# Optimization experiments

Measured on AMD Instinct MI355X. Metric: run time of the kernel, lower is better.

Reference implementation:

```python
import jax, jax.numpy as jnp
import numpy as np

D_MODEL = 2048
N_HEADS = 16
N_KV = 4
HEAD_DIM = 128
SUB = 64
WINDOW = 512
THETA = 10000.0
NEG = jnp.float32(-1e30)


def _rope_tables(seq_len):
    inv_freq = 1.0 / (THETA ** (jnp.arange(0, HEAD_DIM, 2, dtype=jnp.float32) / HEAD_DIM))
    freqs = jnp.arange(seq_len, dtype=jnp.float32)[:, None] * inv_freq[None, :]  # [S, hd/2]
    emb = jnp.concatenate([freqs, freqs], axis=-1)  # [S, hd]
    return jnp.cos(emb), jnp.sin(emb)


def _rotate_half(x):
    x1, x2 = x[..., : HEAD_DIM // 2], x[..., HEAD_DIM // 2 :]
    return jnp.concatenate([-x2, x1], axis=-1)


def _apply_rope(t, cos, sin):
    # t: [B, H, S, hd]; cos/sin: [S, hd]
    c = cos[None, None]
    s = sin[None, None]
    return t * c + _rotate_half(t) * s


def setup_inputs() -> dict:
    key = jax.random.key(0)
    ks = jax.random.split(key, 6)
    B, S = 1, 2048
    std = 0.02
    return {
        "x": jax.random.normal(ks[0], (B, S, D_MODEL), dtype=jnp.float32),
        "Wq": jax.random.normal(ks[1], (D_MODEL, N_HEADS * HEAD_DIM), dtype=jnp.float32) * std,
        "Wk": jax.random.normal(ks[2], (D_MODEL, N_KV * HEAD_DIM), dtype=jnp.float32) * std,
        "Wv": jax.random.normal(ks[3], (D_MODEL, N_KV * HEAD_DIM), dtype=jnp.float32) * std,
        "Wo": jax.random.normal(ks[4], (N_HEADS * HEAD_DIM, D_MODEL), dtype=jnp.float32) * std,
        "lam": jnp.full((N_HEADS,), 0.1, dtype=jnp.float32),
    }


def reference(x, Wq, Wk, Wv, Wo, lam):
    B, S, _ = x.shape
    n_rep = N_HEADS // N_KV

    q = (x @ Wq).reshape(B, S, N_HEADS, HEAD_DIM).transpose(0, 2, 1, 3)  # [B,H,S,hd]
    k = (x @ Wk).reshape(B, S, N_KV, HEAD_DIM).transpose(0, 2, 1, 3)    # [B,KH,S,hd]
    v = (x @ Wv).reshape(B, S, N_KV, HEAD_DIM).transpose(0, 2, 1, 3)

    cos, sin = _rope_tables(S)
    q = _apply_rope(q, cos, sin)
    k = _apply_rope(k, cos, sin)

    # GQA repeat: each kv head replicated n_rep times consecutively
    k = jnp.repeat(k, n_rep, axis=1)  # [B,H,S,hd]
    v = jnp.repeat(v, n_rep, axis=1)

    q1, q2 = q[..., :SUB], q[..., SUB:]
    k1, k2 = k[..., :SUB], k[..., SUB:]
    scale = 1.0 / jnp.sqrt(jnp.float32(SUB))

    s1 = jnp.einsum("bhqd,bhkd->bhqk", q1, k1) * scale
    s2 = jnp.einsum("bhqd,bhkd->bhqk", q2, k2) * scale

    i = jnp.arange(S)[:, None]
    j = jnp.arange(S)[None, :]
    allowed = (j <= i) & (j >= i - WINDOW + 1)  # causal + sliding window
    s1 = jnp.where(allowed[None, None], s1, NEG)
    s2 = jnp.where(allowed[None, None], s2, NEG)

    a1 = jax.nn.softmax(s1.astype(jnp.float32), axis=-1).astype(x.dtype)
    a2 = jax.nn.softmax(s2.astype(jnp.float32), axis=-1).astype(x.dtype)

    diff = jax.nn.relu(a1 - lam[None, :, None, None] * a2)
    diff = diff / (jnp.sum(diff, axis=-1, keepdims=True) + 1e-6)

    out = jnp.einsum("bhqk,bhkd->bhqd", diff, v)  # [B,H,S,hd]
    out = out.transpose(0, 2, 1, 3).reshape(B, S, N_HEADS * HEAD_DIM)
    return out @ Wo
```

## Files before the change

kernel.cpp:

```cpp
#include <hip/hip_runtime.h>
#include <hip/hip_bf16.h>
#include <stdint.h>

typedef __attribute__((ext_vector_type(8))) short short8;
typedef __attribute__((ext_vector_type(4))) float f32x4;
using bf16 = __hip_bfloat16;

#define MFMA16(a, b, c) __builtin_amdgcn_mfma_f32_16x16x32_bf16((a), (b), (c), 0, 0, 0)

#define GLOAD_LDS16(g, l) __builtin_amdgcn_global_load_lds( \
    (const __attribute__((address_space(1))) void*)(g),     \
    (__attribute__((address_space(3))) void*)(l), 16, 0, 0)

__device__ __forceinline__ unsigned packbf2(float lo, float hi) {
  unsigned r;
  asm("v_cvt_pk_bf16_f32 %0, %1, %2" : "=v"(r) : "v"(lo), "v"(hi));
  return r;
}
__device__ __forceinline__ float ex2(float x) {
  float r;
  asm("v_exp_f32 %0, %1" : "=v"(r) : "v"(x));
  return r;
}
__device__ __forceinline__ f32x4 vmax4(f32x4 a, f32x4 b) {
  f32x4 r;
  r[0] = fmaxf(a[0], b[0]); r[1] = fmaxf(a[1], b[1]);
  r[2] = fmaxf(a[2], b[2]); r[3] = fmaxf(a[3], b[3]);
  return r;
}

template <bool EDGE>
__device__ __forceinline__ void p1_update(const f32x4* sv, float& m, float& l,
                                          int kb0, int myq, int lhi) {
  f32x4 t4 = vmax4(vmax4(sv[0], sv[1]), vmax4(sv[2], sv[3]));
  float tm = fmaxf(fmaxf(t4[0], t4[1]), fmaxf(t4[2], t4[3]));
  float nm = fmaxf(m, tm);
  float sc = ex2(m - nm);
  float sum = 0.f;
#pragma unroll
  for (int nt = 0; nt < 4; ++nt) {
    float part = 0.f;
#pragma unroll
    for (int r = 0; r < 4; ++r) {
      float e = ex2(sv[nt][r] - nm);
      if (EDGE) {
        int key = kb0 + nt * 16 + lhi * 4 + r;
        bool ok = (key <= myq) && (key > myq - 512);
        e = ok ? e : 0.f;
      }
      part += e;
    }
    sum += part;
  }
  l = l * sc + sum;
  m = nm;
}

template <bool EDGE>
__device__ __forceinline__ float p2_probs(const f32x4* s1v, const f32x4* s2v,
                                          float m1, float m2, float c2,
                                          int kb0, int myq, int lhi, int l15,
                                          unsigned* pw) {
  float d0 = 0.f, d1 = 0.f;
#pragma unroll
  for (int nt = 0; nt < 4; ++nt) {
    float pr[4];
#pragma unroll
    for (int r = 0; r < 4; ++r) {
      float e1 = ex2(s1v[nt][r] - m1);
      float e2 = ex2(s2v[nt][r] - m2);
      float p = fmaf(-c2, e2, e1);
      p = fmaxf(p, 0.f);
      if (EDGE) {
        int key = kb0 + nt * 16 + lhi * 4 + r;
        bool ok = (key <= myq) && (key > myq - 512);
        p = ok ? p : 0.f;
      }
      pr[r] = p;
      if (r & 1) d1 += p; else d0 += p;
    }
    int pi = l15 * 36 + 8 * nt + 2 * lhi;
    pw[pi]     = packbf2(pr[0], pr[1]);
    pw[pi + 1] = packbf2(pr[2], pr[3]);
  }
  return d0 + d1;
}

__global__ __launch_bounds__(256) void prep_all(const float* __restrict__ x,
                                                const float* __restrict__ Wq,
                                                const float* __restrict__ Wk,
                                                const float* __restrict__ Wv,
                                                const float* __restrict__ Wo,
                                                bf16* __restrict__ xb,
                                                bf16* __restrict__ WqkvFT,
                                                bf16* __restrict__ WoFT)
{
  const int bx = blockIdx.x;
  const int tid = threadIdx.x;
  if (bx >= 80) {
    size_t i = ((size_t)(bx - 80) * 32 + blockIdx.y) * 2048 + tid * 8;
    const float* f = x + i;
    float4 a = *(const float4*)f;
    float4 b = *(const float4*)(f + 4);
    union { bf16 h[8]; short8 s; } u;
    u.h[0] = __float2bfloat16(a.x); u.h[1] = __float2bfloat16(a.y);
    u.h[2] = __float2bfloat16(a.z); u.h[3] = __float2bfloat16(a.w);
    u.h[4] = __float2bfloat16(b.x); u.h[5] = __float2bfloat16(b.y);
    u.h[6] = __float2bfloat16(b.z); u.h[7] = __float2bfloat16(b.w);
    *(short8*)(xb + i) = u.s;
    return;
  }
  const float* W;
  bf16* Wt;
  int N, n0;
  if (bx < 32)      { W = Wq; Wt = WqkvFT; N = 2048; n0 = bx * 64; }
  else if (bx < 40) { W = Wk; Wt = WqkvFT; N = 512;  n0 = 2048 + (bx - 32) * 64; }
  else if (bx < 48) { W = Wv; Wt = WqkvFT; N = 512;  n0 = 2560 + (bx - 40) * 64; }
  else              { W = Wo; Wt = WoFT;   N = 2048; n0 = (bx - 48) * 64; }
  const int nloc0 = (N == 512) ? (n0 - ((n0 >= 2560) ? 2560 : 2048)) : ((bx < 32 || bx >= 48) ? (n0 & 2047) : 0);
  const int k0 = blockIdx.y * 64;

  __shared__ bf16 t[64][72];
#pragma unroll
  for (int pass = 0; pass < 4; ++pass) {
    int r = pass * 16 + (tid >> 4);
    int c = (tid & 15) * 4;
    float4 v = *(const float4*)(W + (size_t)(k0 + r) * N + nloc0 + c);
    t[c + 0][r] = __float2bfloat16(v.x);
    t[c + 1][r] = __float2bfloat16(v.y);
    t[c + 2][r] = __float2bfloat16(v.z);
    t[c + 3][r] = __float2bfloat16(v.w);
  }
  __syncthreads();
#pragma unroll
  for (int pass = 0; pass < 2; ++pass) {
    int n = pass * 32 + (tid >> 3);
    int k8 = (tid & 7) * 8;
    int frag = ((n0 + n) >> 4) * 64 + ((k0 + k8) >> 5);
    int ln = (n & 15) + 16 * ((k8 >> 3) & 3);
    *(short8*)(Wt + (size_t)frag * 512 + ln * 8) = *(const short8*)(&t[n][k8]);
  }
}

__global__ __launch_bounds__(256) void transpose_v(const bf16* __restrict__ QKV,
                                                   bf16* __restrict__ VT)
{
  __shared__ bf16 t[64][72];
  const int tid = threadIdx.x;
  const int k0 = blockIdx.x * 64;
  const int d0 = blockIdx.y * 64;
#pragma unroll
  for (int pass = 0; pass < 2; ++pass) {
    int c = pass * 256 + tid;
    int r = c >> 3, cq = (c & 7) * 8;
    short8 v = *(const short8*)(QKV + (size_t)(k0 + r) * 3072 + 2560 + d0 + cq);
#pragma unroll
    for (int j = 0; j < 8; ++j) t[cq + j][r] = ((const bf16*)&v)[j];
  }
  __syncthreads();
#pragma unroll
  for (int pass = 0; pass < 2; ++pass) {
    int c = pass * 256 + tid;
    int d = c >> 3, kq = (c & 7) * 8;
    *(short8*)(VT + (size_t)(d0 + d) * 2048 + k0 + kq) = *(const short8*)(&t[d][kq]);
  }
}

template <int CF32>
__global__ __launch_bounds__(256) void gemm_ft(const bf16* __restrict__ A,
                                               const bf16* __restrict__ Bft,
                                               void* __restrict__ C,
                                               int M, int N, int K)
{
  __shared__ __align__(16) bf16 As[4][128 * 32];

  const int tid  = threadIdx.x;
  const int lane = tid & 63;
  const int w    = tid >> 6;
  const int wmg  = (w >> 1) * 4;
  const int wng  = (w & 1) * 4;
  const int l15  = lane & 15;
  const int lhi  = lane >> 4;
  const int bm0  = blockIdx.y * 128;
  const int bn0  = blockIdx.x * 128;

  const int srow = lane >> 2;
  const int scol = ((lane & 3) ^ ((lane >> 3) & 3)) * 8;
  const int loff = l15 * 4 + (lhi ^ ((l15 >> 1) & 3));

  const int nkc = K >> 5;
  const bf16* bbase[4];
#pragma unroll
  for (int nt = 0; nt < 4; ++nt)
    bbase[nt] = Bft + ((size_t)((bn0 >> 4) + wng + nt) * nkc) * 512 + lane * 8;

  f32x4 acc[4][4];
  const f32x4 zero4 = {0.f, 0.f, 0.f, 0.f};
#pragma unroll
  for (int i = 0; i < 4; ++i)
#pragma unroll
    for (int j = 0; j < 4; ++j) acc[i][j] = zero4;

  short8 br0[4], br1[4], br2[4], br3[4];

#define GSTAGE_A(buf, kk)                                                          \
  { _Pragma("unroll")                                                              \
    for (int p = 0; p < 2; ++p) {                                                  \
      int s   = (p * 4 + w) * 64 + lane;                                           \
      int row = (p * 4 + w) * 16 + srow;                                           \
      GLOAD_LDS16(A + (size_t)(bm0 + row) * K + (kk) + scol, &As[buf][s * 8]);     \
    } }

#define BLOAD(breg, kc)                                                            \
  { _Pragma("unroll")                                                              \
    for (int nt = 0; nt < 4; ++nt) {                                               \
      asm volatile("global_load_dwordx4 %0, %1, off"                               \
                   : "=v"(breg[nt])                                                \
                   : "v"(bbase[nt] + (size_t)(kc) * 512)                           \
                   : "memory");                                                    \
    } }

#define KSTEP(aslot, breg, wcn, ...)                                               \
  {                                                                                \
    asm volatile("s_waitcnt vmcnt(" #wcn ")" ::: "memory");                        \
    __builtin_amdgcn_s_barrier();                                                  \
    __builtin_amdgcn_sched_barrier(0);                                             \
    __VA_ARGS__                                                                    \
    short8 a_[4];                                                                  \
    _Pragma("unroll")                                                              \
    for (int mt = 0; mt < 4; ++mt)                                                 \
      a_[mt] = *(const short8*)(&As[aslot][((wmg + mt) * 64 + loff) * 8]);         \
    _Pragma("unroll")                                                              \
    for (int mt = 0; mt < 4; ++mt)                                                 \
      _Pragma("unroll")                                                            \
      for (int nt = 0; nt < 4; ++nt)                                               \
        acc[mt][nt] = MFMA16(a_[mt], breg[nt], acc[mt][nt]);                       \
  }

  GSTAGE_A(0, 0);  BLOAD(br0, 0);
  GSTAGE_A(1, 32); BLOAD(br1, 1);
  GSTAGE_A(2, 64); BLOAD(br2, 2);

  for (int t = 0; t < nkc - 4; t += 4) {
    KSTEP(0, br0, 12, GSTAGE_A(3, (t + 3) * 32); BLOAD(br3, t + 3);)
    KSTEP(1, br1, 12, GSTAGE_A(0, (t + 4) * 32); BLOAD(br0, t + 4);)
    KSTEP(2, br2, 12, GSTAGE_A(1, (t + 5) * 32); BLOAD(br1, t + 5);)
    KSTEP(3, br3, 12, GSTAGE_A(2, (t + 6) * 32); BLOAD(br2, t + 6);)
  }
  KSTEP(0, br0, 12, GSTAGE_A(3, (nkc - 1) * 32); BLOAD(br3, nkc - 1);)
  KSTEP(1, br1, 12, )
  KSTEP(2, br2, 6, )
  KSTEP(3, br3, 0, )

#undef GSTAGE_A
#undef BLOAD
#undef KSTEP

#pragma unroll
  for (int mt = 0; mt < 4; ++mt) {
    int row0 = bm0 + (wmg + mt) * 16 + lhi * 4;
#pragma unroll
    for (int nt = 0; nt < 4; ++nt) {
      int col = bn0 + (wng + nt) * 16 + l15;
#pragma unroll
      for (int r = 0; r < 4; ++r) {
        float val = acc[mt][nt][r];
        size_t idx = (size_t)(row0 + r) * N + col;
        if (CF32) ((float*)C)[idx] = val;
        else ((bf16*)C)[idx] = __float2bfloat16(val);
      }
    }
  }
}

__global__ __launch_bounds__(256) void rope2(bf16* __restrict__ QKV)
{
  const int NQ = 2048 * 16 * 8;
  int i = blockIdx.x * blockDim.x + threadIdx.x;
  bf16* base;
  int s, d0;
  float scale;
  if (i < NQ) {
    s = i >> 7;
    int rem = i & 127;
    int h = rem >> 3;
    d0 = (rem & 7) * 8;
    base = QKV + (size_t)s * 3072 + h * 128 + d0;
    scale = 0.180336880111120f;
  } else {
    int j = i - NQ;
    if (j >= 2048 * 4 * 8) return;
    s = j >> 5;
    int rem = j & 31;
    int h = rem >> 3;
    d0 = (rem & 7) * 8;
    base = QKV + (size_t)s * 3072 + 2048 + h * 128 + d0;
    scale = 1.f;
  }
  short8 x1v = *(const short8*)base;
  short8 x2v = *(const short8*)(base + 64);
  union { bf16 h[8]; short8 v; } o1, o2;
#pragma unroll
  for (int e = 0; e < 8; ++e) {
    float inv = __expf(-(float)(d0 + e) * (9.210340371976184f / 64.0f));
    float ang = (float)s * inv;
    float c = __cosf(ang), sn = __sinf(ang);
    union { short s; bf16 b; } u1, u2;
    u1.s = x1v[e]; u2.s = x2v[e];
    float x1 = __bfloat162float(u1.b);
    float x2 = __bfloat162float(u2.b);
    o1.h[e] = __float2bfloat16((x1 * c - x2 * sn) * scale);
    o2.h[e] = __float2bfloat16((x2 * c + x1 * sn) * scale);
  }
  *(short8*)base = o1.v;
  *(short8*)(base + 64) = o2.v;
}

__global__ __launch_bounds__(256) void diff_attn(const bf16* __restrict__ QKV,
                                                 const bf16* __restrict__ VT,
                                                 const float* __restrict__ lam,
                                                 bf16* __restrict__ O)
{
  __shared__ __align__(16) bf16 Kb[2][64 * 128];
  __shared__ __align__(16) bf16 Vb[2][128 * 64];
  __shared__ __align__(16) bf16 Pw[4][16 * 72];

  const int qb   = blockIdx.x;
  const int h    = blockIdx.y;
  const int kvh  = h >> 2;
  const int tid  = threadIdx.x;
  const int lane = tid & 63;
  const int w    = tid >> 6;
  const int l15  = lane & 15;
  const int lhi  = lane >> 4;
  const int qg   = qb * 64 + w * 16;
  const int myq  = qg + l15;
  const float lamv = lam[h];

  const bf16* Kg = QKV + 2048 + (size_t)kvh * 128;
  const bf16* Vg = VT + (size_t)kvh * 128 * 2048;

  short8 qf[4];
  {
    const bf16* qrow = QKV + (size_t)myq * 3072 + h * 128;
#pragma unroll
    for (int c = 0; c < 4; ++c)
      qf[c] = *(const short8*)(qrow + c * 32 + lhi * 8);
  }

  const int t0 = (qb >= 8) ? (qb - 8) : 0;

#define STAGE_K(buf, kbase)                                                     \
  {                                                                             \
    _Pragma("unroll")                                                           \
    for (int p = 0; p < 4; ++p) {                                               \
      int c = p * 256 + tid;                                                    \
      int r = c >> 4, q = c & 15;                                               \
      GLOAD_LDS16(Kg + (size_t)((kbase) + r) * 3072 + ((q ^ (r & 7)) * 8),      \
                  &Kb[buf][c * 8]);                                             \
    }                                                                           \
  }
#define STAGE_V(buf, kbase)                                                     \
  {                                                                             \
    _Pragma("unroll")                                                           \
    for (int p = 0; p < 4; ++p) {                                               \
      int c = p * 256 + tid;                                                    \
      int d = c >> 3, q = c & 7;                                                \
      GLOAD_LDS16(Vg + (size_t)d * 2048 + (kbase) + ((q ^ (d & 7)) * 8),        \
                  &Vb[buf][c * 8]);                                             \
    }                                                                           \
  }
#define KFRAG(buf, nt, qc) \
  (*(const short8*)(&Kb[buf][(((nt) * 16 + l15) * 16 + ((qc) ^ (((nt) * 16 + l15) & 7))) * 8]))
#define VFRAG(buf, n, qc) \
  (*(const short8*)(&Vb[buf][(((n) * 16 + l15) * 8 + ((qc) ^ (((n) * 16 + l15) & 7))) * 8]))
#define QK_TILE(cur)                                            \
  _Pragma("unroll")                                             \
  for (int nt = 0; nt < 4; ++nt) {                              \
    f32x4 s1 = zero4, s2 = zero4;                               \
    s1 = MFMA16(KFRAG(cur, nt, lhi),      qf[0], s1);           \
    s1 = MFMA16(KFRAG(cur, nt, 4 + lhi),  qf[1], s1);           \
    s2 = MFMA16(KFRAG(cur, nt, 8 + lhi),  qf[2], s2);           \
    s2 = MFMA16(KFRAG(cur, nt, 12 + lhi), qf[3], s2);           \
    s1v[nt] = s1; s2v[nt] = s2;                                 \
  }

  const f32x4 zero4 = {0.f, 0.f, 0.f, 0.f};

  float m1 = -1e30f, l1 = 0.f, m2 = -1e30f, l2 = 0.f;
  STAGE_K(0, t0 * 64);
  __syncthreads();
  {
    int cur = 0;
    for (int t = t0; t <= qb; ++t, cur ^= 1) {
      if (t < qb) STAGE_K(cur ^ 1, (t + 1) * 64);
      const int kb0 = t * 64;
      f32x4 s1v[4], s2v[4];
      QK_TILE(cur);
      const bool edge = (t == qb) || (qb >= 8 && t == t0);
      if (edge) {
        p1_update<true>(s1v, m1, l1, kb0, myq, lhi);
        p1_update<true>(s2v, m2, l2, kb0, myq, lhi);
      } else {
        p1_update<false>(s1v, m1, l1, kb0, myq, lhi);
        p1_update<false>(s2v, m2, l2, kb0, myq, lhi);
      }
      __syncthreads();
    }
  }

#pragma unroll
  for (int mk = 16; mk <= 32; mk <<= 1) {
    float pm = __shfl_xor(m1, mk, 64), pl = __shfl_xor(l1, mk, 64);
    float M = fmaxf(m1, pm);
    l1 = l1 * ex2(m1 - M) + pl * ex2(pm - M);
    m1 = M;
    pm = __shfl_xor(m2, mk, 64); pl = __shfl_xor(l2, mk, 64);
    M = fmaxf(m2, pm);
    l2 = l2 * ex2(m2 - M) + pl * ex2(pm - M);
    m2 = M;
  }
  const float c2 = lamv * l1 / l2;

  f32x4 accv[8];
#pragma unroll
  for (int n = 0; n < 8; ++n) accv[n] = zero4;
  float dln = 0.f;

  STAGE_K(0, t0 * 64);
  STAGE_V(0, t0 * 64);
  __syncthreads();
  {
    int cur = 0;
    for (int t = t0; t <= qb; ++t, cur ^= 1) {
      if (t < qb) {
        STAGE_K(cur ^ 1, (t + 1) * 64);
        STAGE_V(cur ^ 1, (t + 1) * 64);
      }
      const int kb0 = t * 64;
      unsigned* pw = (unsigned*)&Pw[w][0];
      f32x4 s1v[4], s2v[4];
      QK_TILE(cur);
      const bool edge = (t == qb) || (qb >= 8 && t == t0);
      if (edge) dln += p2_probs<true>(s1v, s2v, m1, m2, c2, kb0, myq, lhi, l15, pw);
      else      dln += p2_probs<false>(s1v, s2v, m1, m2, c2, kb0, myq, lhi, l15, pw);
#pragma unroll
      for (int kc = 0; kc < 2; ++kc) {
        short8 pa = *(const short8*)(&Pw[w][l15 * 72 + kc * 32 + lhi * 8]);
#pragma unroll
        for (int n = 0; n < 8; ++n)
          accv[n] = MFMA16(pa, VFRAG(cur, n, kc * 4 + lhi), accv[n]);
      }
      __syncthreads();
    }
  }

  dln += __shfl_xor(dln, 16, 64);
  dln += __shfl_xor(dln, 32, 64);

#pragma unroll
  for (int r = 0; r < 4; ++r) {
    int srcq = lhi * 4 + r;
    int src = (lane & 48) | srcq;
    float dq = __shfl(dln, src, 64);
    float lq = __shfl(l1, src, 64);
    float rinv = 1.f / (dq + lq * 1e-6f);
    int qo = qg + srcq;
#pragma unroll
    for (int n = 0; n < 8; ++n) {
      O[(size_t)qo * 2048 + h * 128 + n * 16 + l15] =
          __float2bfloat16(accv[n][r] * rinv);
    }
  }
#undef STAGE_K
#undef STAGE_V
#undef KFRAG
#undef VFRAG
#undef QK_TILE
}

extern "C" void kernel_launch(void* const* d_in, const int* in_sizes, int n_in,
                              void* d_out, int out_size, void* d_ws, size_t ws_size,
                              hipStream_t stream)
{
  const float* x   = (const float*)d_in[0];
  const float* Wq  = (const float*)d_in[1];
  const float* Wk  = (const float*)d_in[2];
  const float* Wv  = (const float*)d_in[3];
  const float* Wo  = (const float*)d_in[4];
  const float* lam = (const float*)d_in[5];

  char* ws = (char*)d_ws;
  bf16* xb     = (bf16*)(ws);
  bf16* WqkvFT = (bf16*)(ws + 8ull  * (1u << 20));
  bf16* WoFT   = (bf16*)(ws + 20ull * (1u << 20));
  bf16* QKV    = (bf16*)(ws + 28ull * (1u << 20));
  bf16* ATT    = (bf16*)(ws + 40ull * (1u << 20));
  bf16* VT     = (bf16*)(ws + 48ull * (1u << 20));

  prep_all<<<dim3(144, 32), 256, 0, stream>>>(x, Wq, Wk, Wv, Wo, xb, WqkvFT, WoFT);
  gemm_ft<0><<<dim3(24, 16), 256, 0, stream>>>(xb, WqkvFT, QKV, 2048, 3072, 2048);
  rope2<<<1280, 256, 0, stream>>>(QKV);
  transpose_v<<<dim3(32, 8), 256, 0, stream>>>(QKV, VT);
  diff_attn<<<dim3(32, 16), 256, 0, stream>>>(QKV, VT, lam, ATT);
  gemm_ft<1><<<dim3(16, 16), 256, 0, stream>>>(ATT, WoFT, d_out, 2048, 2048, 2048);
}
```

Baseline: 116.9 us.

## Store GEMM A operands in MFMA fragment layout and load directly to registers

The x-to-bf16 conversion and the attention output epilogue now write A operands in a pre-fragmented MFMA layout, with the attention output staged through LDS with a swizzle. Both GEMMs can then load A as well as B straight into registers with global_load_dwordx4. This drops the LDS staging, block-wide barriers and LDS reads from the GEMM inner loop. In exchange each wave reloads its A fragments from global/L2 instead of sharing them through LDS, which doubles per-wave global traffic for A, and the attention epilogue gains an extra LDS round trip.

```diff
diff --git a/kernel.cpp b/kernel.cpp
--- a/kernel.cpp
+++ b/kernel.cpp
@@ -91,15 +91,15 @@
                                                 const float* __restrict__ Wk,
                                                 const float* __restrict__ Wv,
                                                 const float* __restrict__ Wo,
-                                                bf16* __restrict__ xb,
+                                                bf16* __restrict__ xbFT,
                                                 bf16* __restrict__ WqkvFT,
                                                 bf16* __restrict__ WoFT)
 {
   const int bx = blockIdx.x;
   const int tid = threadIdx.x;
   if (bx >= 80) {
-    size_t i = ((size_t)(bx - 80) * 32 + blockIdx.y) * 2048 + tid * 8;
-    const float* f = x + i;
+    int row = (bx - 80) * 32 + blockIdx.y;
+    const float* f = x + (size_t)row * 2048 + tid * 8;
     float4 a = *(const float4*)f;
     float4 b = *(const float4*)(f + 4);
     union { bf16 h[8]; short8 s; } u;
@@ -107,7 +107,9 @@
     u.h[2] = __float2bfloat16(a.z); u.h[3] = __float2bfloat16(a.w);
     u.h[4] = __float2bfloat16(b.x); u.h[5] = __float2bfloat16(b.y);
     u.h[6] = __float2bfloat16(b.z); u.h[7] = __float2bfloat16(b.w);
-    *(short8*)(xb + i) = u.s;
+    int frag = (row >> 4) * 64 + (tid >> 2);
+    int ln   = (row & 15) + 16 * (tid & 3);
+    *(short8*)(xbFT + (size_t)frag * 512 + ln * 8) = u.s;
     return;
   }
   const float* W;
@@ -167,13 +169,11 @@
 }
 
 template <int CF32>
-__global__ __launch_bounds__(256) void gemm_ft(const bf16* __restrict__ A,
+__global__ __launch_bounds__(256) void gemm_dd(const bf16* __restrict__ Aft,
                                                const bf16* __restrict__ Bft,
                                                void* __restrict__ C,
                                                int M, int N, int K)
 {
-  __shared__ __align__(16) bf16 As[4][128 * 32];
-
   const int tid  = threadIdx.x;
   const int lane = tid & 63;
   const int w    = tid >> 6;
@@ -183,16 +183,15 @@
   const int lhi  = lane >> 4;
   const int bm0  = blockIdx.y * 128;
   const int bn0  = blockIdx.x * 128;
-
-  const int srow = lane >> 2;
-  const int scol = ((lane & 3) ^ ((lane >> 3) & 3)) * 8;
-  const int loff = l15 * 4 + (lhi ^ ((l15 >> 1) & 3));
-
-  const int nkc = K >> 5;
+  const int nkc  = K >> 5;
+
+  const bf16* abase[4];
   const bf16* bbase[4];
 #pragma unroll
-  for (int nt = 0; nt < 4; ++nt)
-    bbase[nt] = Bft + ((size_t)((bn0 >> 4) + wng + nt) * nkc) * 512 + lane * 8;
+  for (int i = 0; i < 4; ++i) {
+    abase[i] = Aft + ((size_t)((bm0 >> 4) + wmg + i) * nkc) * 512 + lane * 8;
+    bbase[i] = Bft + ((size_t)((bn0 >> 4) + wng + i) * nkc) * 512 + lane * 8;
+  }
 
   f32x4 acc[4][4];
   const f32x4 zero4 = {0.f, 0.f, 0.f, 0.f};
@@ -201,59 +200,46 @@
 #pragma unroll
     for (int j = 0; j < 4; ++j) acc[i][j] = zero4;
 
+  short8 ar0[4], ar1[4], ar2[4], ar3[4];
   short8 br0[4], br1[4], br2[4], br3[4];
 
-#define GSTAGE_A(buf, kk)                                                          \
-  { _Pragma("unroll")                                                              \
-    for (int p = 0; p < 2; ++p) {                                                  \
-      int s   = (p * 4 + w) * 64 + lane;                                           \
-      int row = (p * 4 + w) * 16 + srow;                                           \
-      GLOAD_LDS16(A + (size_t)(bm0 + row) * K + (kk) + scol, &As[buf][s * 8]);     \
-    } }
-
-#define BLOAD(breg, kc)                                                            \
-  { _Pragma("unroll")                                                              \
-    for (int nt = 0; nt < 4; ++nt) {                                               \
-      asm volatile("global_load_dwordx4 %0, %1, off"                               \
-                   : "=v"(breg[nt])                                                \
-                   : "v"(bbase[nt] + (size_t)(kc) * 512)                           \
-                   : "memory");                                                    \
-    } }
-
-#define KSTEP(aslot, breg, wcn, ...)                                               \
-  {                                                                                \
-    asm volatile("s_waitcnt vmcnt(" #wcn ")" ::: "memory");                        \
-    __builtin_amdgcn_s_barrier();                                                  \
-    __builtin_amdgcn_sched_barrier(0);                                             \
-    __VA_ARGS__                                                                    \
-    short8 a_[4];                                                                  \
-    _Pragma("unroll")                                                              \
-    for (int mt = 0; mt < 4; ++mt)                                                 \
-      a_[mt] = *(const short8*)(&As[aslot][((wmg + mt) * 64 + loff) * 8]);         \
-    _Pragma("unroll")                                                              \
-    for (int mt = 0; mt < 4; ++mt)                                                 \
-      _Pragma("unroll")                                                            \
-      for (int nt = 0; nt < 4; ++nt)                                               \
-        acc[mt][nt] = MFMA16(a_[mt], breg[nt], acc[mt][nt]);                       \
-  }
-
-  GSTAGE_A(0, 0);  BLOAD(br0, 0);
-  GSTAGE_A(1, 32); BLOAD(br1, 1);
-  GSTAGE_A(2, 64); BLOAD(br2, 2);
-
-  for (int t = 0; t < nkc - 4; t += 4) {
-    KSTEP(0, br0, 12, GSTAGE_A(3, (t + 3) * 32); BLOAD(br3, t + 3);)
-    KSTEP(1, br1, 12, GSTAGE_A(0, (t + 4) * 32); BLOAD(br0, t + 4);)
-    KSTEP(2, br2, 12, GSTAGE_A(1, (t + 5) * 32); BLOAD(br1, t + 5);)
-    KSTEP(3, br3, 12, GSTAGE_A(2, (t + 6) * 32); BLOAD(br2, t + 6);)
-  }
-  KSTEP(0, br0, 12, GSTAGE_A(3, (nkc - 1) * 32); BLOAD(br3, nkc - 1);)
-  KSTEP(1, br1, 12, )
-  KSTEP(2, br2, 6, )
-  KSTEP(3, br3, 0, )
-
-#undef GSTAGE_A
-#undef BLOAD
+#define LOADS(ar, br, kc)                                                           \
+  { _Pragma("unroll")                                                               \
+    for (int i = 0; i < 4; ++i)                                                     \
+      asm volatile("global_load_dwordx4 %0, %1, off"                                \
+                   : "=v"(ar[i]) : "v"(abase[i] + (size_t)(kc) * 512) : "memory");  \
+    _Pragma("unroll")                                                               \
+    for (int i = 0; i < 4; ++i)                                                     \
+      asm volatile("global_load_dwordx4 %0, %1, off"                                \
+                   : "=v"(br[i]) : "v"(bbase[i] + (size_t)(kc) * 512) : "memory");  \
+  }
+
+#define KSTEP(ar, br, wcn, ...)                                                     \
+  { asm volatile("s_waitcnt vmcnt(" #wcn ")" ::: "memory");                         \
+    __builtin_amdgcn_sched_barrier(0);                                              \
+    __VA_ARGS__                                                                     \
+    _Pragma("unroll")                                                               \
+    for (int mt = 0; mt < 4; ++mt)                                                  \
+      _Pragma("unroll")                                                             \
+      for (int nt = 0; nt < 4; ++nt)                                                \
+        acc[mt][nt] = MFMA16(ar[mt], br[nt], acc[mt][nt]);                          \
+  }
+
+  LOADS(ar0, br0, 0);
+  LOADS(ar1, br1, 1);
+  LOADS(ar2, br2, 2);
+
+  for (int t = 0; t + 8 <= nkc; t += 4) {
+    KSTEP(ar0, br0, 16, LOADS(ar3, br3, t + 3);)
+    KSTEP(ar1, br1, 16, LOADS(ar0, br0, t + 4);)
+    KSTEP(ar2, br2, 16, LOADS(ar1, br1, t + 5);)
+    KSTEP(ar3, br3, 16, LOADS(ar2, br2, t + 6);)
+  }
+  KSTEP(ar0, br0, 16, LOADS(ar3, br3, nkc - 1);)
+  KSTEP(ar1, br1, 16, )
+  KSTEP(ar2, br2, 8, )
+  KSTEP(ar3, br3, 0, )
+#undef LOADS
 #undef KSTEP
 
 #pragma unroll
@@ -319,7 +305,7 @@
 __global__ __launch_bounds__(256) void diff_attn(const bf16* __restrict__ QKV,
                                                  const bf16* __restrict__ VT,
                                                  const float* __restrict__ lam,
-                                                 bf16* __restrict__ O)
+                                                 bf16* __restrict__ ATTft)
 {
   __shared__ __align__(16) bf16 Kb[2][64 * 128];
   __shared__ __align__(16) bf16 Vb[2][128 * 64];
@@ -458,6 +444,7 @@
   dln += __shfl_xor(dln, 16, 64);
   dln += __shfl_xor(dln, 32, 64);
 
+  bf16* L = &Kb[0][0];
 #pragma unroll
   for (int r = 0; r < 4; ++r) {
     int srcq = lhi * 4 + r;
@@ -465,12 +452,22 @@
     float dq = __shfl(dln, src, 64);
     float lq = __shfl(l1, src, 64);
     float rinv = 1.f / (dq + lq * 1e-6f);
-    int qo = qg + srcq;
+    int mloc = w * 16 + srcq;
+    int swz = mloc & 15;
 #pragma unroll
     for (int n = 0; n < 8; ++n) {
-      O[(size_t)qo * 2048 + h * 128 + n * 16 + l15] =
-          __float2bfloat16(accv[n][r] * rinv);
+      int cc = n * 2 + (l15 >> 3);
+      L[(mloc * 16 + (cc ^ swz)) * 8 + (l15 & 7)] = __float2bfloat16(accv[n][r] * rinv);
     }
+  }
+  __syncthreads();
+#pragma unroll
+  for (int p = 0; p < 4; ++p) {
+    int m = p * 16 + l15;
+    int ccr = w * 4 + lhi;
+    short8 v = *(const short8*)(&L[(m * 16 + (ccr ^ l15)) * 8]);
+    size_t frag = (size_t)(qb * 4 + p) * 64 + h * 4 + w;
+    *(short8*)(ATTft + frag * 512 + lane * 8) = v;
   }
 #undef STAGE_K
 #undef STAGE_V
@@ -491,17 +488,17 @@
   const float* lam = (const float*)d_in[5];
 
   char* ws = (char*)d_ws;
-  bf16* xb     = (bf16*)(ws);
+  bf16* xbFT   = (bf16*)(ws);
   bf16* WqkvFT = (bf16*)(ws + 8ull  * (1u << 20));
   bf16* WoFT   = (bf16*)(ws + 20ull * (1u << 20));
   bf16* QKV    = (bf16*)(ws + 28ull * (1u << 20));
-  bf16* ATT    = (bf16*)(ws + 40ull * (1u << 20));
+  bf16* ATTft  = (bf16*)(ws + 40ull * (1u << 20));
   bf16* VT     = (bf16*)(ws + 48ull * (1u << 20));
 
-  prep_all<<<dim3(144, 32), 256, 0, stream>>>(x, Wq, Wk, Wv, Wo, xb, WqkvFT, WoFT);
-  gemm_ft<0><<<dim3(24, 16), 256, 0, stream>>>(xb, WqkvFT, QKV, 2048, 3072, 2048);
+  prep_all<<<dim3(144, 32), 256, 0, stream>>>(x, Wq, Wk, Wv, Wo, xbFT, WqkvFT, WoFT);
+  gemm_dd<0><<<dim3(24, 16), 256, 0, stream>>>(xbFT, WqkvFT, QKV, 2048, 3072, 2048);
   rope2<<<1280, 256, 0, stream>>>(QKV);
   transpose_v<<<dim3(32, 8), 256, 0, stream>>>(QKV, VT);
-  diff_attn<<<dim3(32, 16), 256, 0, stream>>>(QKV, VT, lam, ATT);
-  gemm_ft<1><<<dim3(16, 16), 256, 0, stream>>>(ATT, WoFT, d_out, 2048, 2048, 2048);
-}
+  diff_attn<<<dim3(32, 16), 256, 0, stream>>>(QKV, VT, lam, ATTft);
+  gemm_dd<1><<<dim3(16, 16), 256, 0, stream>>>(ATTft, WoFT, d_out, 2048, 2048, 2048);
+}
```

After: 120.2 us. 2.9% more time.

## Fuse RoPE and V transpose into QKV GEMM epilogue

Applied to the files above, without the earlier changes.

The QKV projection GEMM now stages its accumulator tile in shared memory and applies RoPE (with the query scale) directly before writing bf16 Q/K. For V columns it writes the transposed V layout directly. This removes two separate kernel launches and their global read/write passes over QKV. The cost is extra epilogue work and syncs in the GEMM, and V is no longer written to QKV (diff_attn reads VT only).

```diff
diff --git a/kernel.cpp b/kernel.cpp
--- a/kernel.cpp
+++ b/kernel.cpp
@@ -142,34 +142,11 @@
   }
 }
 
-__global__ __launch_bounds__(256) void transpose_v(const bf16* __restrict__ QKV,
-                                                   bf16* __restrict__ VT)
-{
-  __shared__ bf16 t[64][72];
-  const int tid = threadIdx.x;
-  const int k0 = blockIdx.x * 64;
-  const int d0 = blockIdx.y * 64;
-#pragma unroll
-  for (int pass = 0; pass < 2; ++pass) {
-    int c = pass * 256 + tid;
-    int r = c >> 3, cq = (c & 7) * 8;
-    short8 v = *(const short8*)(QKV + (size_t)(k0 + r) * 3072 + 2560 + d0 + cq);
-#pragma unroll
-    for (int j = 0; j < 8; ++j) t[cq + j][r] = ((const bf16*)&v)[j];
-  }
-  __syncthreads();
-#pragma unroll
-  for (int pass = 0; pass < 2; ++pass) {
-    int c = pass * 256 + tid;
-    int d = c >> 3, kq = (c & 7) * 8;
-    *(short8*)(VT + (size_t)(d0 + d) * 2048 + k0 + kq) = *(const short8*)(&t[d][kq]);
-  }
-}
-
-template <int CF32>
+template <int EPI>
 __global__ __launch_bounds__(256) void gemm_ft(const bf16* __restrict__ A,
                                                const bf16* __restrict__ Bft,
                                                void* __restrict__ C,
+                                               bf16* __restrict__ VTp,
                                                int M, int N, int K)
 {
   __shared__ __align__(16) bf16 As[4][128 * 32];
@@ -251,69 +228,97 @@
   KSTEP(1, br1, 12, )
   KSTEP(2, br2, 6, )
   KSTEP(3, br3, 0, )
-
 #undef GSTAGE_A
 #undef BLOAD
 #undef KSTEP
 
-#pragma unroll
-  for (int mt = 0; mt < 4; ++mt) {
-    int row0 = bm0 + (wmg + mt) * 16 + lhi * 4;
-#pragma unroll
-    for (int nt = 0; nt < 4; ++nt) {
-      int col = bn0 + (wng + nt) * 16 + l15;
-#pragma unroll
-      for (int r = 0; r < 4; ++r) {
-        float val = acc[mt][nt][r];
-        size_t idx = (size_t)(row0 + r) * N + col;
-        if (CF32) ((float*)C)[idx] = val;
-        else ((bf16*)C)[idx] = __float2bfloat16(val);
-      }
-    }
-  }
-}
-
-__global__ __launch_bounds__(256) void rope2(bf16* __restrict__ QKV)
-{
-  const int NQ = 2048 * 16 * 8;
-  int i = blockIdx.x * blockDim.x + threadIdx.x;
-  bf16* base;
-  int s, d0;
-  float scale;
-  if (i < NQ) {
-    s = i >> 7;
-    int rem = i & 127;
-    int h = rem >> 3;
-    d0 = (rem & 7) * 8;
-    base = QKV + (size_t)s * 3072 + h * 128 + d0;
-    scale = 0.180336880111120f;
+  if (EPI == 1) {
+#pragma unroll
+    for (int mt = 0; mt < 4; ++mt) {
+      int row0 = bm0 + (wmg + mt) * 16 + lhi * 4;
+#pragma unroll
+      for (int nt = 0; nt < 4; ++nt) {
+        int col = bn0 + (wng + nt) * 16 + l15;
+#pragma unroll
+        for (int r = 0; r < 4; ++r)
+          ((float*)C)[(size_t)(row0 + r) * N + col] = acc[mt][nt][r];
+      }
+    }
+    return;
+  }
+
+  __syncthreads();
+  if (bn0 < 2560) {
+    float* Lf = (float*)&As[0][0];
+    const float scale = (bn0 < 2048) ? 0.180336880111120f : 1.0f;
+#pragma unroll
+    for (int c = 0; c < 2; ++c) {
+      if ((w >> 1) == c) {
+#pragma unroll
+        for (int mt = 0; mt < 4; ++mt)
+#pragma unroll
+          for (int nt = 0; nt < 4; ++nt) {
+            int col = (wng + nt) * 16 + l15;
+#pragma unroll
+            for (int r = 0; r < 4; ++r)
+              Lf[(mt * 16 + lhi * 4 + r) * 128 + col] = acc[mt][nt][r];
+          }
+      }
+      __syncthreads();
+      {
+        int rloc = tid >> 2;
+        int dg = (tid & 3) * 16;
+        int s = bm0 + c * 64 + rloc;
+        bf16* orow = (bf16*)C + (size_t)s * N + bn0;
+        union { bf16 h[16]; short8 v[2]; } o1, o2;
+#pragma unroll
+        for (int e = 0; e < 16; ++e) {
+          int d = dg + e;
+          float inv = __expf(-(float)d * (9.210340371976184f / 64.0f));
+          float ang = (float)s * inv;
+          float cs = __cosf(ang), sn = __sinf(ang);
+          float x1 = Lf[rloc * 128 + d];
+          float x2 = Lf[rloc * 128 + d + 64];
+          o1.h[e] = __float2bfloat16((x1 * cs - x2 * sn) * scale);
+          o2.h[e] = __float2bfloat16((x2 * cs + x1 * sn) * scale);
+        }
+        *(short8*)(orow + dg)      = o1.v[0];
+        *(short8*)(orow + dg + 8)  = o1.v[1];
+        *(short8*)(orow + dg + 64) = o2.v[0];
+        *(short8*)(orow + dg + 72) = o2.v[1];
+      }
+      __syncthreads();
+    }
   } else {
-    int j = i - NQ;
-    if (j >= 2048 * 4 * 8) return;
-    s = j >> 5;
-    int rem = j & 31;
-    int h = rem >> 3;
-    d0 = (rem & 7) * 8;
-    base = QKV + (size_t)s * 3072 + 2048 + h * 128 + d0;
-    scale = 1.f;
-  }
-  short8 x1v = *(const short8*)base;
-  short8 x2v = *(const short8*)(base + 64);
-  union { bf16 h[8]; short8 v; } o1, o2;
-#pragma unroll
-  for (int e = 0; e < 8; ++e) {
-    float inv = __expf(-(float)(d0 + e) * (9.210340371976184f / 64.0f));
-    float ang = (float)s * inv;
-    float c = __cosf(ang), sn = __sinf(ang);
-    union { short s; bf16 b; } u1, u2;
-    u1.s = x1v[e]; u2.s = x2v[e];
-    float x1 = __bfloat162float(u1.b);
-    float x2 = __bfloat162float(u2.b);
-    o1.h[e] = __float2bfloat16((x1 * c - x2 * sn) * scale);
-    o2.h[e] = __float2bfloat16((x2 * c + x1 * sn) * scale);
-  }
-  *(short8*)base = o1.v;
-  *(short8*)(base + 64) = o2.v;
+    bf16* Lb = &As[0][0];
+#pragma unroll
+    for (int cc = 0; cc < 2; ++cc) {
+      if ((w & 1) == cc) {
+#pragma unroll
+        for (int mt = 0; mt < 4; ++mt)
+#pragma unroll
+          for (int nt = 0; nt < 4; ++nt) {
+            int colloc = nt * 16 + l15;
+#pragma unroll
+            for (int r = 0; r < 4; ++r) {
+              int key = (wmg + mt) * 16 + lhi * 4 + r;
+              Lb[colloc * 136 + key] = __float2bfloat16(acc[mt][nt][r]);
+            }
+          }
+      }
+      __syncthreads();
+      {
+        int dl = tid >> 2;
+        int kq = (tid & 3) * 32;
+        int dim = (bn0 - 2560) + cc * 64 + dl;
+        bf16* vrow = VTp + (size_t)dim * 2048 + bm0 + kq;
+#pragma unroll
+        for (int j = 0; j < 4; ++j)
+          *(short8*)(vrow + j * 8) = *(const short8*)(&Lb[dl * 136 + kq + j * 8]);
+      }
+      __syncthreads();
+    }
+  }
 }
 
 __global__ __launch_bounds__(256) void diff_attn(const bf16* __restrict__ QKV,
@@ -499,9 +504,7 @@
   bf16* VT     = (bf16*)(ws + 48ull * (1u << 20));
 
   prep_all<<<dim3(144, 32), 256, 0, stream>>>(x, Wq, Wk, Wv, Wo, xb, WqkvFT, WoFT);
-  gemm_ft<0><<<dim3(24, 16), 256, 0, stream>>>(xb, WqkvFT, QKV, 2048, 3072, 2048);
-  rope2<<<1280, 256, 0, stream>>>(QKV);
-  transpose_v<<<dim3(32, 8), 256, 0, stream>>>(QKV, VT);
+  gemm_ft<0><<<dim3(24, 16), 256, 0, stream>>>(xb, WqkvFT, QKV, VT, 2048, 3072, 2048);
   diff_attn<<<dim3(32, 16), 256, 0, stream>>>(QKV, VT, lam, ATT);
-  gemm_ft<1><<<dim3(16, 16), 256, 0, stream>>>(ATT, WoFT, d_out, 2048, 2048, 2048);
-}
+  gemm_ft<1><<<dim3(16, 16), 256, 0, stream>>>(ATT, WoFT, d_out, nullptr, 2048, 2048, 2048);
+}
```

New measurement: 111.5 us. -4.6%, faster.
